# Performance work log

Hardware: AMD Instinct MI355X
Metric: run time of the kernel (lower is better)

The kernel has to match this reference:

```python
import jax, jax.numpy as jnp
import numpy as np

EPS_T = 1e-4    # min ray t to count as a hit
BIG = 1e10      # sentinel for 'no hit'
NRM_EPS = 1e-12 # F.normalize eps


def _normalize(x):
    n = jnp.linalg.norm(x, axis=-1, keepdims=True)
    return x / jnp.maximum(n, NRM_EPS)


def _to_local(d, n):
    # Build orthonormal frame (s, t, n) from normal n (Duff et al. branchless),
    # then express d in that local frame: Frame.to_local.
    sign = jnp.where(n[..., 2] >= 0.0, 1.0, -1.0)
    a = -1.0 / (sign + n[..., 2])
    b = n[..., 0] * n[..., 1] * a
    s = jnp.stack([1.0 + sign * n[..., 0] ** 2 * a, sign * b, -sign * n[..., 0]], axis=-1)
    t = jnp.stack([b, sign + n[..., 1] ** 2 * a, -n[..., 1]], axis=-1)
    return jnp.stack([jnp.sum(d * s, -1), jnp.sum(d * t, -1), jnp.sum(d * n, -1)], axis=-1)


def setup_inputs() -> dict:
    key = jax.random.key(0)
    k = jax.random.split(key, 6)
    N, S, L = 524288, 128, 64
    ray_o = jax.random.normal(k[0], (N, 3), jnp.float32) * 5.0
    ray_d = jax.random.normal(k[1], (N, 3), jnp.float32)
    centers = jax.random.normal(k[2], (S, 3), jnp.float32) * 5.0
    radii = 0.5 + jax.random.uniform(k[3], (S,), jnp.float32)
    light_pos = jax.random.normal(k[4], (L, 3), jnp.float32) * 10.0
    light_idx = jax.random.randint(k[5], (N,), 0, L, jnp.int32)
    return {"ray_o": ray_o, "ray_d": ray_d, "centers": centers, "radii": radii,
            "light_pos": light_pos, "light_idx": light_idx}


def reference(ray_o, ray_d, centers, radii, light_pos, light_idx):
    # --- shapes.intersect(rays): brute-force nearest ray-sphere hit ---
    d = _normalize(ray_d)                                   # [N,3]
    od = jnp.sum(ray_o * d, -1)                             # [N]
    b = od[:, None] - jnp.einsum('nk,sk->ns', d, centers)   # [N,S]
    c = (jnp.sum(ray_o ** 2, -1)[:, None]
         - 2.0 * jnp.einsum('nk,sk->ns', ray_o, centers)
         + jnp.sum(centers ** 2, -1)[None, :]
         - radii[None, :] ** 2)                              # [N,S]
    disc = b * b - c
    t = -b - jnp.sqrt(jnp.maximum(disc, 0.0))
    valid = (disc > 0.0) & (t > EPS_T)
    t = jnp.where(valid, t, BIG)
    tmin = jnp.min(t, axis=1)                               # [N]
    sidx = jnp.argmin(t, axis=1)                            # [N]
    active = tmin < BIG                                     # [N] bool
    p = ray_o + tmin[:, None] * d                           # hit point [N,3]
    n = _normalize(p - centers[sidx])                       # surface normal [N,3]
    # --- sample_emitter_dir_wo_isect: direction to the sampled point light ---
    ds_d = light_pos[light_idx] - p                         # [N,3]
    # --- local-frame transform + normalize + where glue ---
    local = _to_local(ds_d, n)
    results = jnp.where(active[:, None], (_normalize(local) + 1.0) / 2.0,
                        jnp.zeros_like(ds_d))
    return (1.0 + results) / 2.0, active
```

## Files before the change

kernel.cpp:

```cpp
#include <hip/hip_runtime.h>
#include <math.h>

#define EPS_T 1e-4f
#define BIG 1e10f
#define NRM_EPS 1e-12f

typedef float v2f __attribute__((ext_vector_type(2)));

#define PF0 \
  "ds_read_b128 v[40:43], %[lda] offset:0\n\t" \
  "ds_read_b128 v[44:47], %[lda] offset:16\n\t" \
  "v_add_u32 %[lda], 32, %[lda]\n\t"
#define PF1 \
  "ds_read_b128 v[48:51], %[lda] offset:0\n\t" \
  "ds_read_b128 v[52:55], %[lda] offset:16\n\t" \
  "v_add_u32 %[lda], 32, %[lda]\n\t"

#define PBODY(W, CX, CY, CZ, CWN, PF) \
  W \
  "v_pk_mul_f32 v[32:33], %[dz2], " CZ "\n\t" \
  "v_pk_mul_f32 v[34:35], %[oz2], " CZ "\n\t" \
  "v_pk_fma_f32 v[32:33], %[dy2], " CY ", v[32:33]\n\t" \
  "v_pk_fma_f32 v[34:35], %[oy2], " CY ", v[34:35]\n\t" \
  "v_pk_fma_f32 v[32:33], %[dx2], " CX ", v[32:33]\n\t" \
  "v_pk_fma_f32 v[34:35], %[ox2], " CX ", v[34:35]\n\t" \
  "v_pk_add_f32 v[36:37], v[32:33], %[nod2]\n\t" \
  "v_pk_fma_f32 v[38:39], v[34:35], %[two2], %[noo2]\n\t" \
  "v_pk_add_f32 v[38:39], v[38:39], " CWN "\n\t" \
  PF \
  "v_pk_fma_f32 v[38:39], v[36:37], v[36:37], v[38:39]\n\t" \
  "v_sqrt_f32 v56, v38\n\t" \
  "v_sqrt_f32 v57, v39\n\t" \
  "v_sub_f32 v56, v36, v56\n\t" \
  "v_sub_f32 v57, v37, v57\n\t" \
  "v_cmp_lt_f32 vcc, %[eps], v56\n\t" \
  "v_cmp_gt_f32 s[20:21], %[tme], v56\n\t" \
  "s_and_b64 vcc, vcc, s[20:21]\n\t" \
  "v_cndmask_b32 %[tme], %[tme], v56, vcc\n\t" \
  "v_cndmask_b32 %[ide], %[ide], %[vj], vcc\n\t" \
  "v_cmp_lt_f32 vcc, %[eps], v57\n\t" \
  "v_cmp_gt_f32 s[20:21], %[tmo], v57\n\t" \
  "s_and_b64 vcc, vcc, s[20:21]\n\t" \
  "v_cndmask_b32 %[tmo], %[tmo], v57, vcc\n\t" \
  "v_cndmask_b32 %[ido], %[ido], %[vj], vcc\n\t" \
  "v_add_u32 %[vj], 1, %[vj]\n\t"

__global__ __launch_bounds__(256) void illum_kernel(
    const float* __restrict__ ray_o,
    const float* __restrict__ ray_d,
    const float* __restrict__ centers,
    const float* __restrict__ radii,
    const float* __restrict__ light_pos,
    const int*   __restrict__ light_idx,
    float* __restrict__ out,
    int N)
{
    __shared__ float4 tab[128];

    const int tid = threadIdx.x;
    if (tid < 64) {
        float x0 = centers[6 * tid + 0], y0 = centers[6 * tid + 1], z0 = centers[6 * tid + 2];
        float x1 = centers[6 * tid + 3], y1 = centers[6 * tid + 4], z1 = centers[6 * tid + 5];
        float r0 = radii[2 * tid + 0],   r1 = radii[2 * tid + 1];
        float w0 = x0 * x0 + y0 * y0 + z0 * z0 - r0 * r0;
        float w1 = x1 * x1 + y1 * y1 + z1 * z1 - r1 * r1;
        tab[2 * tid + 0] = make_float4(x0, x1, y0, y1);
        tab[2 * tid + 1] = make_float4(z0, z1, -w0, -w1);
    }
    __syncthreads();

    const int i = blockIdx.x * blockDim.x + tid;
    if (i >= N) return;

    float ox = ray_o[3 * i + 0], oy = ray_o[3 * i + 1], oz = ray_o[3 * i + 2];
    float dx = ray_d[3 * i + 0], dy = ray_d[3 * i + 1], dz = ray_d[3 * i + 2];

    float dn  = sqrtf(dx * dx + dy * dy + dz * dz);
    float din = 1.0f / fmaxf(dn, NRM_EPS);
    dx *= din; dy *= din; dz *= din;

    const float od = ox * dx + oy * dy + oz * dz;
    const float oo = ox * ox + oy * oy + oz * oz;

    v2f dx2 = {dx, dx}, dy2 = {dy, dy}, dz2 = {dz, dz};
    v2f ox2 = {ox, ox}, oy2 = {oy, oy}, oz2 = {oz, oz};
    v2f nod2 = {-od, -od};
    v2f noo2 = {-oo, -oo};
    v2f two2 = {2.0f, 2.0f};

    float tme = BIG, tmo = BIG;
    int ide = 0, ido = 0, vj = 0;
    unsigned lda = (unsigned)(size_t)&tab[0];

    asm volatile(
        "s_waitcnt lgkmcnt(0)\n\t"
        PF0
        PF1
        ".rept 31\n\t"
        PBODY("s_waitcnt lgkmcnt(2)\n\t", "v[40:41]", "v[42:43]", "v[44:45]", "v[46:47]", PF0)
        PBODY("s_waitcnt lgkmcnt(2)\n\t", "v[48:49]", "v[50:51]", "v[52:53]", "v[54:55]", PF1)
        ".endr\n\t"
        PBODY("s_waitcnt lgkmcnt(2)\n\t", "v[40:41]", "v[42:43]", "v[44:45]", "v[46:47]", "")
        PBODY("s_waitcnt lgkmcnt(0)\n\t", "v[48:49]", "v[50:51]", "v[52:53]", "v[54:55]", "")
        : [tme]"+v"(tme), [tmo]"+v"(tmo), [ide]"+v"(ide), [ido]"+v"(ido),
          [vj]"+v"(vj), [lda]"+v"(lda)
        : [dx2]"v"(dx2), [dy2]"v"(dy2), [dz2]"v"(dz2),
          [ox2]"v"(ox2), [oy2]"v"(oy2), [oz2]"v"(oz2),
          [nod2]"v"(nod2), [noo2]"v"(noo2), [two2]"v"(two2),
          [eps]"s"(1e-4f)
        : "v32","v33","v34","v35","v36","v37","v38","v39",
          "v40","v41","v42","v43","v44","v45","v46","v47",
          "v48","v49","v50","v51","v52","v53","v54","v55","v56","v57",
          "s20","s21","vcc","scc","memory");

    int iE = 2 * ide, iO = 2 * ido + 1;
    bool ow = (tmo < tme) | ((tmo == tme) & (iO < iE));
    float tmin = ow ? tmo : tme;
    int   sidx = ow ? iO  : iE;

    const bool active = (tmin < BIG);

    float px = fmaf(tmin, dx, ox);
    float py = fmaf(tmin, dy, oy);
    float pz = fmaf(tmin, dz, oz);

    float4 ab = tab[2 * (sidx >> 1) + 0];
    float4 zw = tab[2 * (sidx >> 1) + 1];
    float cbx = (sidx & 1) ? ab.y : ab.x;
    float cby = (sidx & 1) ? ab.w : ab.z;
    float cbz = (sidx & 1) ? zw.y : zw.x;
    float nx = px - cbx, ny = py - cby, nz = pz - cbz;
    float nn  = sqrtf(nx * nx + ny * ny + nz * nz);
    float nin = 1.0f / fmaxf(nn, NRM_EPS);
    nx *= nin; ny *= nin; nz *= nin;

    int li = light_idx[i];
    float dsx = light_pos[3 * li + 0] - px;
    float dsy = light_pos[3 * li + 1] - py;
    float dsz = light_pos[3 * li + 2] - pz;

    float sgn = (nz >= 0.0f) ? 1.0f : -1.0f;
    float a   = -1.0f / (sgn + nz);
    float bb  = nx * ny * a;
    float sx = 1.0f + sgn * nx * nx * a, sy = sgn * bb,          sz = -sgn * nx;
    float tx = bb,                       ty = sgn + ny * ny * a, tz = -ny;

    float l0 = dsx * sx + dsy * sy + dsz * sz;
    float l1 = dsx * tx + dsy * ty + dsz * tz;
    float l2 = dsx * nx + dsy * ny + dsz * nz;
    float ln  = sqrtf(l0 * l0 + l1 * l1 + l2 * l2);
    float lin = 1.0f / fmaxf(ln, NRM_EPS);

    float r0 = active ? (l0 * lin + 1.0f) * 0.5f : 0.0f;
    float r1 = active ? (l1 * lin + 1.0f) * 0.5f : 0.0f;
    float r2 = active ? (l2 * lin + 1.0f) * 0.5f : 0.0f;

    out[3 * i + 0] = (1.0f + r0) * 0.5f;
    out[3 * i + 1] = (1.0f + r1) * 0.5f;
    out[3 * i + 2] = (1.0f + r2) * 0.5f;
    out[(size_t)3 * N + i] = active ? 1.0f : 0.0f;
}

extern "C" void kernel_launch(void* const* d_in, const int* in_sizes, int n_in,
                              void* d_out, int out_size, void* d_ws, size_t ws_size,
                              hipStream_t stream) {
    const float* ray_o     = (const float*)d_in[0];
    const float* ray_d     = (const float*)d_in[1];
    const float* centers   = (const float*)d_in[2];
    const float* radii     = (const float*)d_in[3];
    const float* light_pos = (const float*)d_in[4];
    const int*   light_idx = (const int*)d_in[5];
    float* out = (float*)d_out;

    const int N = in_sizes[0] / 3;

    const int block = 256;
    const int grid  = (N + block - 1) / block;
    illum_kernel<<<grid, block, 0, stream>>>(ray_o, ray_d, centers, radii,
                                             light_pos, light_idx, out, N);
}
```

Baseline: 32.14 us.

## Process two rays per thread to reuse LDS sphere loads across rays

```diff
diff --git a/kernel.cpp b/kernel.cpp
--- a/kernel.cpp
+++ b/kernel.cpp
@@ -16,36 +16,66 @@
   "ds_read_b128 v[52:55], %[lda] offset:16\n\t" \
   "v_add_u32 %[lda], 32, %[lda]\n\t"
 
-#define PBODY(W, CX, CY, CZ, CWN, PF) \
+#define PBODY2(W, CX, CY, CZ, CWN, PF) \
   W \
-  "v_pk_mul_f32 v[32:33], %[dz2], " CZ "\n\t" \
-  "v_pk_mul_f32 v[34:35], %[oz2], " CZ "\n\t" \
-  "v_pk_fma_f32 v[32:33], %[dy2], " CY ", v[32:33]\n\t" \
-  "v_pk_fma_f32 v[34:35], %[oy2], " CY ", v[34:35]\n\t" \
-  "v_pk_fma_f32 v[32:33], %[dx2], " CX ", v[32:33]\n\t" \
-  "v_pk_fma_f32 v[34:35], %[ox2], " CX ", v[34:35]\n\t" \
-  "v_pk_add_f32 v[36:37], v[32:33], %[nod2]\n\t" \
-  "v_pk_fma_f32 v[38:39], v[34:35], %[two2], %[noo2]\n\t" \
+   \
+  "v_pk_mul_f32 v[32:33], %[dzA], " CZ "\n\t" \
+  "v_pk_mul_f32 v[34:35], %[ozA], " CZ "\n\t" \
+  "v_pk_fma_f32 v[32:33], %[dyA], " CY ", v[32:33]\n\t" \
+  "v_pk_fma_f32 v[34:35], %[oyA], " CY ", v[34:35]\n\t" \
+  "v_pk_fma_f32 v[32:33], %[dxA], " CX ", v[32:33]\n\t" \
+  "v_pk_fma_f32 v[34:35], %[oxA], " CX ", v[34:35]\n\t" \
+   \
+  "v_pk_mul_f32 v[58:59], %[dzB], " CZ "\n\t" \
+  "v_pk_mul_f32 v[60:61], %[ozB], " CZ "\n\t" \
+  "v_pk_fma_f32 v[58:59], %[dyB], " CY ", v[58:59]\n\t" \
+  "v_pk_fma_f32 v[60:61], %[oyB], " CY ", v[60:61]\n\t" \
+  "v_pk_fma_f32 v[58:59], %[dxB], " CX ", v[58:59]\n\t" \
+  "v_pk_fma_f32 v[60:61], %[oxB], " CX ", v[60:61]\n\t" \
+   \
+  "v_pk_add_f32 v[36:37], v[32:33], %[nodA]\n\t" \
+  "v_pk_fma_f32 v[38:39], v[34:35], %[two2], %[nooA]\n\t" \
   "v_pk_add_f32 v[38:39], v[38:39], " CWN "\n\t" \
-  PF \
   "v_pk_fma_f32 v[38:39], v[36:37], v[36:37], v[38:39]\n\t" \
   "v_sqrt_f32 v56, v38\n\t" \
   "v_sqrt_f32 v57, v39\n\t" \
+   \
+  "v_pk_add_f32 v[62:63], v[58:59], %[nodB]\n\t" \
+  "v_pk_fma_f32 v[64:65], v[60:61], %[two2], %[nooB]\n\t" \
+  "v_pk_add_f32 v[64:65], v[64:65], " CWN "\n\t" \
+  "v_pk_fma_f32 v[64:65], v[62:63], v[62:63], v[64:65]\n\t" \
+  "v_sqrt_f32 v66, v64\n\t" \
+  "v_sqrt_f32 v67, v65\n\t" \
+  PF \
+   \
   "v_sub_f32 v56, v36, v56\n\t" \
   "v_sub_f32 v57, v37, v57\n\t" \
   "v_cmp_lt_f32 vcc, %[eps], v56\n\t" \
-  "v_cmp_gt_f32 s[20:21], %[tme], v56\n\t" \
-  "s_and_b64 vcc, vcc, s[20:21]\n\t" \
-  "v_cndmask_b32 %[tme], %[tme], v56, vcc\n\t" \
-  "v_cndmask_b32 %[ide], %[ide], %[vj], vcc\n\t" \
+  "v_cmp_gt_f32 s[20:21], %[tmeA], v56\n\t" \
+  "s_and_b64 vcc, vcc, s[20:21]\n\t" \
+  "v_cndmask_b32 %[tmeA], %[tmeA], v56, vcc\n\t" \
+  "v_cndmask_b32 %[ideA], %[ideA], %[vj], vcc\n\t" \
   "v_cmp_lt_f32 vcc, %[eps], v57\n\t" \
-  "v_cmp_gt_f32 s[20:21], %[tmo], v57\n\t" \
-  "s_and_b64 vcc, vcc, s[20:21]\n\t" \
-  "v_cndmask_b32 %[tmo], %[tmo], v57, vcc\n\t" \
-  "v_cndmask_b32 %[ido], %[ido], %[vj], vcc\n\t" \
+  "v_cmp_gt_f32 s[20:21], %[tmoA], v57\n\t" \
+  "s_and_b64 vcc, vcc, s[20:21]\n\t" \
+  "v_cndmask_b32 %[tmoA], %[tmoA], v57, vcc\n\t" \
+  "v_cndmask_b32 %[idoA], %[idoA], %[vj], vcc\n\t" \
+   \
+  "v_sub_f32 v66, v62, v66\n\t" \
+  "v_sub_f32 v67, v63, v67\n\t" \
+  "v_cmp_lt_f32 vcc, %[eps], v66\n\t" \
+  "v_cmp_gt_f32 s[20:21], %[tmeB], v66\n\t" \
+  "s_and_b64 vcc, vcc, s[20:21]\n\t" \
+  "v_cndmask_b32 %[tmeB], %[tmeB], v66, vcc\n\t" \
+  "v_cndmask_b32 %[ideB], %[ideB], %[vj], vcc\n\t" \
+  "v_cmp_lt_f32 vcc, %[eps], v67\n\t" \
+  "v_cmp_gt_f32 s[20:21], %[tmoB], v67\n\t" \
+  "s_and_b64 vcc, vcc, s[20:21]\n\t" \
+  "v_cndmask_b32 %[tmoB], %[tmoB], v67, vcc\n\t" \
+  "v_cndmask_b32 %[idoB], %[idoB], %[vj], vcc\n\t" \
   "v_add_u32 %[vj], 1, %[vj]\n\t"
 
-__global__ __launch_bounds__(256) void illum_kernel(
+__global__ __launch_bounds__(256, 4) void illum_kernel(
     const float* __restrict__ ray_o,
     const float* __restrict__ ray_d,
     const float* __restrict__ centers,
@@ -69,27 +99,44 @@
     }
     __syncthreads();
 
-    const int i = blockIdx.x * blockDim.x + tid;
-    if (i >= N) return;
-
-    float ox = ray_o[3 * i + 0], oy = ray_o[3 * i + 1], oz = ray_o[3 * i + 2];
-    float dx = ray_d[3 * i + 0], dy = ray_d[3 * i + 1], dz = ray_d[3 * i + 2];
-
-    float dn  = sqrtf(dx * dx + dy * dy + dz * dz);
-    float din = 1.0f / fmaxf(dn, NRM_EPS);
-    dx *= din; dy *= din; dz *= din;
-
-    const float od = ox * dx + oy * dy + oz * dz;
-    const float oo = ox * ox + oy * oy + oz * oz;
-
-    v2f dx2 = {dx, dx}, dy2 = {dy, dy}, dz2 = {dz, dz};
-    v2f ox2 = {ox, ox}, oy2 = {oy, oy}, oz2 = {oz, oz};
-    v2f nod2 = {-od, -od};
-    v2f noo2 = {-oo, -oo};
+    const int ti = blockIdx.x * blockDim.x + tid;
+    const int rA = 2 * ti;
+    const int rB = rA + 1;
+    if (rA >= N) return;
+    const bool hasB = (rB < N);
+
+    const float2* o2 = (const float2*)ray_o;
+    const float2* d2 = (const float2*)ray_d;
+    float2 oa = o2[3 * ti + 0], ob = o2[3 * ti + 1], oc = o2[3 * ti + 2];
+    float2 da = d2[3 * ti + 0], db = d2[3 * ti + 1], dc = d2[3 * ti + 2];
+
+    float oxA = oa.x, oyA = oa.y, ozA = ob.x;
+    float oxB = ob.y, oyB = oc.x, ozB = oc.y;
+    float dxA = da.x, dyA = da.y, dzA = db.x;
+    float dxB = db.y, dyB = dc.x, dzB = dc.y;
+
+    float dnA  = sqrtf(dxA * dxA + dyA * dyA + dzA * dzA);
+    float dinA = 1.0f / fmaxf(dnA, NRM_EPS);
+    dxA *= dinA; dyA *= dinA; dzA *= dinA;
+    float dnB  = sqrtf(dxB * dxB + dyB * dyB + dzB * dzB);
+    float dinB = 1.0f / fmaxf(dnB, NRM_EPS);
+    dxB *= dinB; dyB *= dinB; dzB *= dinB;
+
+    const float odA = oxA * dxA + oyA * dyA + ozA * dzA;
+    const float ooA = oxA * oxA + oyA * oyA + ozA * ozA;
+    const float odB = oxB * dxB + oyB * dyB + ozB * dzB;
+    const float ooB = oxB * oxB + oyB * oyB + ozB * ozB;
+
+    v2f dxA2 = {dxA, dxA}, dyA2 = {dyA, dyA}, dzA2 = {dzA, dzA};
+    v2f oxA2 = {oxA, oxA}, oyA2 = {oyA, oyA}, ozA2 = {ozA, ozA};
+    v2f nodA2 = {-odA, -odA}, nooA2 = {-ooA, -ooA};
+    v2f dxB2 = {dxB, dxB}, dyB2 = {dyB, dyB}, dzB2 = {dzB, dzB};
+    v2f oxB2 = {oxB, oxB}, oyB2 = {oyB, oyB}, ozB2 = {ozB, ozB};
+    v2f nodB2 = {-odB, -odB}, nooB2 = {-ooB, -ooB};
     v2f two2 = {2.0f, 2.0f};
 
-    float tme = BIG, tmo = BIG;
-    int ide = 0, ido = 0, vj = 0;
+    float tmeA = BIG, tmoA = BIG, tmeB = BIG, tmoB = BIG;
+    int ideA = 0, idoA = 0, ideB = 0, idoB = 0, vj = 0;
     unsigned lda = (unsigned)(size_t)&tab[0];
 
     asm volatile(
@@ -97,68 +144,83 @@
         PF0
         PF1
         ".rept 31\n\t"
-        PBODY("s_waitcnt lgkmcnt(2)\n\t", "v[40:41]", "v[42:43]", "v[44:45]", "v[46:47]", PF0)
-        PBODY("s_waitcnt lgkmcnt(2)\n\t", "v[48:49]", "v[50:51]", "v[52:53]", "v[54:55]", PF1)
+        PBODY2("s_waitcnt lgkmcnt(2)\n\t", "v[40:41]", "v[42:43]", "v[44:45]", "v[46:47]", PF0)
+        PBODY2("s_waitcnt lgkmcnt(2)\n\t", "v[48:49]", "v[50:51]", "v[52:53]", "v[54:55]", PF1)
         ".endr\n\t"
-        PBODY("s_waitcnt lgkmcnt(2)\n\t", "v[40:41]", "v[42:43]", "v[44:45]", "v[46:47]", "")
-        PBODY("s_waitcnt lgkmcnt(0)\n\t", "v[48:49]", "v[50:51]", "v[52:53]", "v[54:55]", "")
-        : [tme]"+v"(tme), [tmo]"+v"(tmo), [ide]"+v"(ide), [ido]"+v"(ido),
+        PBODY2("s_waitcnt lgkmcnt(2)\n\t", "v[40:41]", "v[42:43]", "v[44:45]", "v[46:47]", "")
+        PBODY2("s_waitcnt lgkmcnt(0)\n\t", "v[48:49]", "v[50:51]", "v[52:53]", "v[54:55]", "")
+        : [tmeA]"+v"(tmeA), [tmoA]"+v"(tmoA), [ideA]"+v"(ideA), [idoA]"+v"(idoA),
+          [tmeB]"+v"(tmeB), [tmoB]"+v"(tmoB), [ideB]"+v"(ideB), [idoB]"+v"(idoB),
           [vj]"+v"(vj), [lda]"+v"(lda)
-        : [dx2]"v"(dx2), [dy2]"v"(dy2), [dz2]"v"(dz2),
-          [ox2]"v"(ox2), [oy2]"v"(oy2), [oz2]"v"(oz2),
-          [nod2]"v"(nod2), [noo2]"v"(noo2), [two2]"v"(two2),
-          [eps]"s"(1e-4f)
+        : [dxA]"v"(dxA2), [dyA]"v"(dyA2), [dzA]"v"(dzA2),
+          [oxA]"v"(oxA2), [oyA]"v"(oyA2), [ozA]"v"(ozA2),
+          [nodA]"v"(nodA2), [nooA]"v"(nooA2),
+          [dxB]"v"(dxB2), [dyB]"v"(dyB2), [dzB]"v"(dzB2),
+          [oxB]"v"(oxB2), [oyB]"v"(oyB2), [ozB]"v"(ozB2),
+          [nodB]"v"(nodB2), [nooB]"v"(nooB2),
+          [two2]"v"(two2), [eps]"s"(1e-4f)
         : "v32","v33","v34","v35","v36","v37","v38","v39",
           "v40","v41","v42","v43","v44","v45","v46","v47",
-          "v48","v49","v50","v51","v52","v53","v54","v55","v56","v57",
+          "v48","v49","v50","v51","v52","v53","v54","v55",
+          "v56","v57","v58","v59","v60","v61","v62","v63",
+          "v64","v65","v66","v67",
           "s20","s21","vcc","scc","memory");
 
-    int iE = 2 * ide, iO = 2 * ido + 1;
-    bool ow = (tmo < tme) | ((tmo == tme) & (iO < iE));
-    float tmin = ow ? tmo : tme;
-    int   sidx = ow ? iO  : iE;
-
-    const bool active = (tmin < BIG);
-
-    float px = fmaf(tmin, dx, ox);
-    float py = fmaf(tmin, dy, oy);
-    float pz = fmaf(tmin, dz, oz);
-
-    float4 ab = tab[2 * (sidx >> 1) + 0];
-    float4 zw = tab[2 * (sidx >> 1) + 1];
-    float cbx = (sidx & 1) ? ab.y : ab.x;
-    float cby = (sidx & 1) ? ab.w : ab.z;
-    float cbz = (sidx & 1) ? zw.y : zw.x;
-    float nx = px - cbx, ny = py - cby, nz = pz - cbz;
-    float nn  = sqrtf(nx * nx + ny * ny + nz * nz);
-    float nin = 1.0f / fmaxf(nn, NRM_EPS);
-    nx *= nin; ny *= nin; nz *= nin;
-
-    int li = light_idx[i];
-    float dsx = light_pos[3 * li + 0] - px;
-    float dsy = light_pos[3 * li + 1] - py;
-    float dsz = light_pos[3 * li + 2] - pz;
-
-    float sgn = (nz >= 0.0f) ? 1.0f : -1.0f;
-    float a   = -1.0f / (sgn + nz);
-    float bb  = nx * ny * a;
-    float sx = 1.0f + sgn * nx * nx * a, sy = sgn * bb,          sz = -sgn * nx;
-    float tx = bb,                       ty = sgn + ny * ny * a, tz = -ny;
-
-    float l0 = dsx * sx + dsy * sy + dsz * sz;
-    float l1 = dsx * tx + dsy * ty + dsz * tz;
-    float l2 = dsx * nx + dsy * ny + dsz * nz;
-    float ln  = sqrtf(l0 * l0 + l1 * l1 + l2 * l2);
-    float lin = 1.0f / fmaxf(ln, NRM_EPS);
-
-    float r0 = active ? (l0 * lin + 1.0f) * 0.5f : 0.0f;
-    float r1 = active ? (l1 * lin + 1.0f) * 0.5f : 0.0f;
-    float r2 = active ? (l2 * lin + 1.0f) * 0.5f : 0.0f;
-
-    out[3 * i + 0] = (1.0f + r0) * 0.5f;
-    out[3 * i + 1] = (1.0f + r1) * 0.5f;
-    out[3 * i + 2] = (1.0f + r2) * 0.5f;
-    out[(size_t)3 * N + i] = active ? 1.0f : 0.0f;
+    auto shade = [&](float ox, float oy, float oz, float dx, float dy, float dz,
+                     float tme, float tmo, int ide, int ido, int ray, float* res) {
+        int iE = 2 * ide, iO = 2 * ido + 1;
+        bool ow = (tmo < tme) | ((tmo == tme) & (iO < iE));
+        float tmin = ow ? tmo : tme;
+        int   sidx = ow ? iO  : iE;
+        const bool active = (tmin < BIG);
+
+        float px = fmaf(tmin, dx, ox);
+        float py = fmaf(tmin, dy, oy);
+        float pz = fmaf(tmin, dz, oz);
+        float4 ab = tab[2 * (sidx >> 1) + 0];
+        float4 zw = tab[2 * (sidx >> 1) + 1];
+        float cbx = (sidx & 1) ? ab.y : ab.x;
+        float cby = (sidx & 1) ? ab.w : ab.z;
+        float cbz = (sidx & 1) ? zw.y : zw.x;
+        float nx = px - cbx, ny = py - cby, nz = pz - cbz;
+        float nn  = sqrtf(nx * nx + ny * ny + nz * nz);
+        float nin = 1.0f / fmaxf(nn, NRM_EPS);
+        nx *= nin; ny *= nin; nz *= nin;
+        int li = light_idx[ray];
+        float dsx = light_pos[3 * li + 0] - px;
+        float dsy = light_pos[3 * li + 1] - py;
+        float dsz = light_pos[3 * li + 2] - pz;
+        float sgn = (nz >= 0.0f) ? 1.0f : -1.0f;
+        float a   = -1.0f / (sgn + nz);
+        float bb  = nx * ny * a;
+        float sx = 1.0f + sgn * nx * nx * a, sy = sgn * bb,          sz = -sgn * nx;
+        float tx = bb,                       ty = sgn + ny * ny * a, tz = -ny;
+        float l0 = dsx * sx + dsy * sy + dsz * sz;
+        float l1 = dsx * tx + dsy * ty + dsz * tz;
+        float l2 = dsx * nx + dsy * ny + dsz * nz;
+        float ln  = sqrtf(l0 * l0 + l1 * l1 + l2 * l2);
+        float lin = 1.0f / fmaxf(ln, NRM_EPS);
+        res[0] = active ? ((l0 * lin + 1.0f) * 0.5f + 1.0f) * 0.5f : 0.5f;
+        res[1] = active ? ((l1 * lin + 1.0f) * 0.5f + 1.0f) * 0.5f : 0.5f;
+        res[2] = active ? ((l2 * lin + 1.0f) * 0.5f + 1.0f) * 0.5f : 0.5f;
+        res[3] = active ? 1.0f : 0.0f;
+    };
+
+    float resA[4], resB[4] = {0.5f, 0.5f, 0.5f, 0.0f};
+    shade(oxA, oyA, ozA, dxA, dyA, dzA, tmeA, tmoA, ideA, idoA, rA, resA);
+    if (hasB) shade(oxB, oyB, ozB, dxB, dyB, dzB, tmeB, tmoB, ideB, idoB, rB, resB);
+
+    float2* ro = (float2*)(out + 6 * (size_t)ti);
+    ro[0] = make_float2(resA[0], resA[1]);
+    if (hasB) {
+        ro[1] = make_float2(resA[2], resB[0]);
+        ro[2] = make_float2(resB[1], resB[2]);
+        float2* ao = (float2*)(out + 3 * (size_t)N + 2 * (size_t)ti);
+        ao[0] = make_float2(resA[3], resB[3]);
+    } else {
+        out[6 * (size_t)ti + 2] = resA[2];
+        out[3 * (size_t)N + rA] = resA[3];
+    }
 }
 
 extern "C" void kernel_launch(void* const* d_in, const int* in_sizes, int n_in,
@@ -174,8 +236,9 @@
 
     const int N = in_sizes[0] / 3;
 
+    const int NP = (N + 1) / 2;
     const int block = 256;
-    const int grid  = (N + block - 1) / block;
+    const int grid  = (NP + block - 1) / block;
     illum_kernel<<<grid, block, 0, stream>>>(ray_o, ray_d, centers, radii,
                                              light_pos, light_idx, out, N);
 }
```

New measurement: 33.69 us. 1.05x slower.
